# Kernel tuning notes

Hardware: AMD Instinct MI355X
Metric: run time of the kernel (lower is better)

The kernel has to match this reference:

```python
import jax, jax.numpy as jnp
import numpy as np


def setup_inputs() -> dict:
    key = jax.random.key(0)
    k1, k2 = jax.random.split(key)
    s = jax.random.normal(k1, (8192, 512), dtype=jnp.float32)
    t = jax.random.normal(k2, (8192, 512), dtype=jnp.float32)
    return {"s": s, "t": t}


def reference(s, t):
    # Pairwise squared Euclidean distance: dist[i, j] = ||t[j] - s[i]||^2
    # Expressed via the identity ||s||^2 + ||t||^2 - 2 s @ t^T to avoid
    # materializing the [n, q, d] broadcast intermediate of the original.
    s_sq = jnp.sum(s * s, axis=1)  # [n]
    t_sq = jnp.sum(t * t, axis=1)  # [q]
    cross = jnp.einsum('nd,qd->nq', s, t)  # [n, q]
    dist = s_sq[:, None] + t_sq[None, :] - 2.0 * cross
    return dist
```

## Files before the change

kernel.cpp:

```cpp
#include <hip/hip_runtime.h>
#include <hip/hip_bf16.h>
#include <stdint.h>


typedef __attribute__((ext_vector_type(8))) short short8v;
typedef __attribute__((ext_vector_type(4))) float f32x4;

static __device__ __forceinline__ unsigned short f32_to_bf16_rne(float f) {
    unsigned int u = __float_as_uint(f);
    unsigned int lsb = (u >> 16) & 1u;
    u += 0x7fffu + lsb;
    return (unsigned short)(u >> 16);
}

static __device__ __forceinline__ void async_load16(const void* g, void* l) {
    __builtin_amdgcn_global_load_lds(
        (const __attribute__((address_space(1))) void*)g,
        (__attribute__((address_space(3))) void*)l,
        16, 0, 0);
}

__global__ __launch_bounds__(256) void prep_kernel(const float* __restrict__ x,
                                                   unsigned short* __restrict__ xb,
                                                   float* __restrict__ nrm,
                                                   float scale) {
    const int tid  = threadIdx.x;
    const int wid  = tid >> 6;
    const int lane = tid & 63;
    const int row  = blockIdx.x * 4 + wid;
    const float* xr = x + (size_t)row * 512;

    float4 v0 = ((const float4*)xr)[lane * 2 + 0];
    float4 v1 = ((const float4*)xr)[lane * 2 + 1];

    float ss = v0.x * v0.x + v0.y * v0.y + v0.z * v0.z + v0.w * v0.w
             + v1.x * v1.x + v1.y * v1.y + v1.z * v1.z + v1.w * v1.w;
#pragma unroll
    for (int off = 32; off > 0; off >>= 1) ss += __shfl_down(ss, off, 64);
    if (lane == 0) nrm[row] = ss;

    unsigned short u[8];
    float vals[8] = {v0.x, v0.y, v0.z, v0.w, v1.x, v1.y, v1.z, v1.w};
#pragma unroll
    for (int e = 0; e < 8; ++e) u[e] = f32_to_bf16_rne(vals[e] * scale);
    unsigned int w0 = (unsigned)u[0] | ((unsigned)u[1] << 16);
    unsigned int w1 = (unsigned)u[2] | ((unsigned)u[3] << 16);
    unsigned int w2 = (unsigned)u[4] | ((unsigned)u[5] << 16);
    unsigned int w3 = (unsigned)u[6] | ((unsigned)u[7] << 16);
    uint4 pk = make_uint4(w0, w1, w2, w3);
    ((uint4*)(xb + (size_t)row * 512))[lane] = pk;
}

#define TILE 128
#define BK 64

__global__ __launch_bounds__(256) void dist_mfma(const unsigned short* __restrict__ sb,
                                                 const unsigned short* __restrict__ tb,
                                                 const float* __restrict__ ssq,
                                                 const float* __restrict__ tsq,
                                                 float* __restrict__ out,
                                                 int N, int Q, int D) {
    __shared__ unsigned short lds_a[TILE * BK];
    __shared__ unsigned short lds_b[TILE * BK];

    const int tid  = threadIdx.x;
    const int wid  = tid >> 6;
    const int lane = tid & 63;
    const int quad = lane >> 4;
    const int r    = lane & 15;

    const int bid = blockIdx.x;
    const int nBm = N / TILE, nBn = Q / TILE;
    int bm, bn;
    if ((nBm & 7) == 0 && (nBn & 7) == 0) {
        const int super = bid >> 6, within = bid & 63;
        const int spr = nBn >> 3;
        const int sm = super / spr, sn = super % spr;
        bm = (sm << 3) + (within >> 3);
        bn = (sn << 3) + (within & 7);
    } else {
        bm = bid / nBn;
        bn = bid - bm * nBn;
    }

    const int m_w = (wid & 1) * 64;
    const int n_w = (wid >> 1) * 64;

    f32x4 acc[4][4];
#pragma unroll
    for (int a = 0; a < 4; ++a)
#pragma unroll
        for (int b = 0; b < 4; ++b) acc[a][b] = (f32x4){0.f, 0.f, 0.f, 0.f};

    const unsigned short* gA[4];
    const unsigned short* gB[4];
    unsigned short* lA[4];
    unsigned short* lB[4];
#pragma unroll
    for (int i = 0; i < 4; ++i) {
        const int p    = i * 256 + tid;
        const int row  = p >> 3;
        const int gch  = (tid & 7) ^ (row & 7);
        gA[i] = sb + (size_t)(bm * TILE + row) * D + gch * 8;
        gB[i] = tb + (size_t)(bn * TILE + row) * D + gch * 8;
        lA[i] = lds_a + (i * 256 + wid * 64) * 8;
        lB[i] = lds_b + (i * 256 + wid * 64) * 8;
    }

    for (int k0 = 0; k0 < D; k0 += BK) {
        __syncthreads();
#pragma unroll
        for (int i = 0; i < 4; ++i) {
            async_load16(gA[i] + k0, lA[i]);
            async_load16(gB[i] + k0, lB[i]);
        }
        __syncthreads();

#pragma unroll
        for (int ks = 0; ks < 2; ++ks) {
            short8v aF[4], bF[4];
#pragma unroll
            for (int im = 0; im < 4; ++im) {
                const int row = m_w + im * 16 + r;
                const int cp  = (ks * 4 + quad) ^ (row & 7);
                aF[im] = *(const short8v*)(lds_a + row * BK + cp * 8);
            }
#pragma unroll
            for (int in = 0; in < 4; ++in) {
                const int row = n_w + in * 16 + r;
                const int cp  = (ks * 4 + quad) ^ (row & 7);
                bF[in] = *(const short8v*)(lds_b + row * BK + cp * 8);
            }
#pragma unroll
            for (int im = 0; im < 4; ++im)
#pragma unroll
                for (int in = 0; in < 4; ++in)
                    acc[im][in] = __builtin_amdgcn_mfma_f32_16x16x32_bf16(
                        aF[im], bF[in], acc[im][in], 0, 0, 0);
        }
    }

    const int gm = bm * TILE + m_w;
    const int gn = bn * TILE + n_w;
    float tq[4];
#pragma unroll
    for (int in = 0; in < 4; ++in) tq[in] = tsq[gn + in * 16 + r];
#pragma unroll
    for (int im = 0; im < 4; ++im) {
#pragma unroll
        for (int j = 0; j < 4; ++j) {
            const int i = gm + im * 16 + quad * 4 + j;
            const float sv = ssq[i];
            float* orow = out + (size_t)i * (size_t)Q + gn;
#pragma unroll
            for (int in = 0; in < 4; ++in)
                __builtin_nontemporal_store(sv + tq[in] + acc[im][in][j],
                                            &orow[in * 16 + r]);
        }
    }
}

__global__ void dist_fallback(const float* __restrict__ s, const float* __restrict__ t,
                              float* __restrict__ out, int N, int Q, int D) {
    __shared__ float ls[16][17], lt[16][17];
    const int tj = threadIdx.x, ti = threadIdx.y;
    const int i = blockIdx.y * 16 + ti, j = blockIdx.x * 16 + tj;
    float cross = 0.f, ssq = 0.f, tsq = 0.f;
    for (int k0 = 0; k0 < D; k0 += 16) {
        __syncthreads();
        ls[ti][tj] = s[(size_t)(blockIdx.y * 16 + ti) * D + k0 + tj];
        lt[ti][tj] = t[(size_t)(blockIdx.x * 16 + ti) * D + k0 + tj];
        __syncthreads();
#pragma unroll
        for (int kk = 0; kk < 16; ++kk) {
            float a = ls[ti][kk], b = lt[tj][kk];
            cross += a * b; ssq += a * a; tsq += b * b;
        }
    }
    out[(size_t)i * Q + j] = ssq + tsq - 2.f * cross;
}

extern "C" void kernel_launch(void* const* d_in, const int* in_sizes, int n_in,
                              void* d_out, int out_size, void* d_ws, size_t ws_size,
                              hipStream_t stream) {
    const float* s = (const float*)d_in[0];
    const float* t = (const float*)d_in[1];
    float* out = (float*)d_out;
    const int D = 512;
    const int N = in_sizes[0] / D;
    const int Q = in_sizes[1] / D;

    const size_t need = ((size_t)N + (size_t)Q) * D * sizeof(unsigned short)
                      + ((size_t)N + (size_t)Q) * sizeof(float);

    if (ws_size >= need && D == 512 && (N % TILE) == 0 && (Q % TILE) == 0) {
        unsigned short* sb = (unsigned short*)d_ws;
        unsigned short* tb = sb + (size_t)N * D;
        float* ssq = (float*)(tb + (size_t)Q * D);
        float* tsq = ssq + N;
        prep_kernel<<<N / 4, 256, 0, stream>>>(s, sb, ssq, -2.0f);
        prep_kernel<<<Q / 4, 256, 0, stream>>>(t, tb, tsq, 1.0f);
        const int blocks = (N / TILE) * (Q / TILE);
        dist_mfma<<<blocks, 256, 0, stream>>>(sb, tb, ssq, tsq, out, N, Q, D);
    } else {
        dim3 g(Q / 16, N / 16), b(16, 16);
        dist_fallback<<<g, b, 0, stream>>>(s, t, out, N, Q, D);
    }
}
```

Measured before the change: 347.9 us.

## Use 256x256 tiles with a 4-slot async LDS ring and prefetch depth two

Grows the block tile from 128x128 to 256x256 with 512 threads, so each wave computes a 128x64 sub-tile. The K step shrinks to 32, and global-to-LDS loads go into a 4-slot ring buffer issued two stages ahead. Explicit vmcnt waits plus one barrier per step replace the previous load-then-sync pattern, which stalled on every K step. MFMA priority is raised during the compute section; the risk is 128KB of LDS limiting occupancy to one block per CU, plus higher register use.

```diff
diff --git a/kernel.cpp b/kernel.cpp
--- a/kernel.cpp
+++ b/kernel.cpp
@@ -51,26 +51,30 @@
     ((uint4*)(xb + (size_t)row * 512))[lane] = pk;
 }
 
-#define TILE 128
-#define BK 64
-
-__global__ __launch_bounds__(256) void dist_mfma(const unsigned short* __restrict__ sb,
-                                                 const unsigned short* __restrict__ tb,
-                                                 const float* __restrict__ ssq,
-                                                 const float* __restrict__ tsq,
-                                                 float* __restrict__ out,
-                                                 int N, int Q, int D) {
-    __shared__ unsigned short lds_a[TILE * BK];
-    __shared__ unsigned short lds_b[TILE * BK];
+#define BM 256
+#define BK 32
+#define NSLOT 4
+
+__global__ __launch_bounds__(512, 2) void dist_mfma(const unsigned short* __restrict__ sb,
+                                                    const unsigned short* __restrict__ tb,
+                                                    const float* __restrict__ ssq,
+                                                    const float* __restrict__ tsq,
+                                                    float* __restrict__ out,
+                                                    int N, int Q, int D) {
+    __shared__ __align__(16) unsigned short lds[2 * NSLOT * 256 * 32];
 
     const int tid  = threadIdx.x;
     const int wid  = tid >> 6;
     const int lane = tid & 63;
     const int quad = lane >> 4;
     const int r    = lane & 15;
+    const int wr   = wid >> 2;
+    const int wc   = wid & 3;
+    const int m_w  = wr * 128;
+    const int n_w  = wc * 64;
 
     const int bid = blockIdx.x;
-    const int nBm = N / TILE, nBn = Q / TILE;
+    const int nBm = N / BM, nBn = Q / BM;
     int bm, bn;
     if ((nBm & 7) == 0 && (nBn & 7) == 0) {
         const int super = bid >> 6, within = bid & 63;
@@ -83,70 +87,83 @@
         bn = bid - bm * nBn;
     }
 
-    const int m_w = (wid & 1) * 64;
-    const int n_w = (wid >> 1) * 64;
-
-    f32x4 acc[4][4];
-#pragma unroll
-    for (int a = 0; a < 4; ++a)
+    f32x4 acc[8][4];
+#pragma unroll
+    for (int a = 0; a < 8; ++a)
 #pragma unroll
         for (int b = 0; b < 4; ++b) acc[a][b] = (f32x4){0.f, 0.f, 0.f, 0.f};
 
-    const unsigned short* gA[4];
-    const unsigned short* gB[4];
-    unsigned short* lA[4];
-    unsigned short* lB[4];
-#pragma unroll
-    for (int i = 0; i < 4; ++i) {
-        const int p    = i * 256 + tid;
-        const int row  = p >> 3;
-        const int gch  = (tid & 7) ^ (row & 7);
-        gA[i] = sb + (size_t)(bm * TILE + row) * D + gch * 8;
-        gB[i] = tb + (size_t)(bn * TILE + row) * D + gch * 8;
-        lA[i] = lds_a + (i * 256 + wid * 64) * 8;
-        lB[i] = lds_b + (i * 256 + wid * 64) * 8;
-    }
-
-    for (int k0 = 0; k0 < D; k0 += BK) {
-        __syncthreads();
-#pragma unroll
-        for (int i = 0; i < 4; ++i) {
-            async_load16(gA[i] + k0, lA[i]);
-            async_load16(gB[i] + k0, lB[i]);
-        }
-        __syncthreads();
-
-#pragma unroll
-        for (int ks = 0; ks < 2; ++ks) {
-            short8v aF[4], bF[4];
-#pragma unroll
-            for (int im = 0; im < 4; ++im) {
-                const int row = m_w + im * 16 + r;
-                const int cp  = (ks * 4 + quad) ^ (row & 7);
-                aF[im] = *(const short8v*)(lds_a + row * BK + cp * 8);
-            }
-#pragma unroll
-            for (int in = 0; in < 4; ++in) {
-                const int row = n_w + in * 16 + r;
-                const int cp  = (ks * 4 + quad) ^ (row & 7);
-                bF[in] = *(const short8v*)(lds_b + row * BK + cp * 8);
-            }
-#pragma unroll
-            for (int im = 0; im < 4; ++im)
-#pragma unroll
-                for (int in = 0; in < 4; ++in)
-                    acc[im][in] = __builtin_amdgcn_mfma_f32_16x16x32_bf16(
-                        aF[im], bF[in], acc[im][in], 0, 0, 0);
-        }
-    }
-
-    const int gm = bm * TILE + m_w;
-    const int gn = bn * TILE + n_w;
+    const unsigned short* gA[2];
+    const unsigned short* gB[2];
+    unsigned short* lA[2];
+    unsigned short* lB[2];
+#pragma unroll
+    for (int i = 0; i < 2; ++i) {
+        const int p   = i * 512 + tid;
+        const int row = p >> 2;
+        const int gch = (p & 3) ^ (row & 3);
+        gA[i] = sb + (size_t)(bm * BM + row) * D + gch * 8;
+        gB[i] = tb + (size_t)(bn * BM + row) * D + gch * 8;
+        lA[i] = lds + (i * 512 + wid * 64) * 8;
+        lB[i] = lds + NSLOT * 8192 + (i * 512 + wid * 64) * 8;
+    }
+
+#define STAGE(t, s) do { const int k0_ = (t) * BK;                  \
+        async_load16(gA[0] + k0_, lA[0] + (s) * 8192);              \
+        async_load16(gB[0] + k0_, lB[0] + (s) * 8192);              \
+        async_load16(gA[1] + k0_, lA[1] + (s) * 8192);              \
+        async_load16(gB[1] + k0_, lB[1] + (s) * 8192); } while (0)
+
+    STAGE(0, 0);
+    STAGE(1, 1);
+
+    const int NT = D / BK;
+    for (int t = 0; t < NT; ++t) {
+        if (t + 2 < NT) STAGE(t + 2, (t + 2) & 3);
+        if (t < NT - 2) {
+            asm volatile("s_waitcnt vmcnt(8) lgkmcnt(0)" ::: "memory");
+        } else if (t == NT - 2) {
+            asm volatile("s_waitcnt vmcnt(4) lgkmcnt(0)" ::: "memory");
+        } else {
+            asm volatile("s_waitcnt vmcnt(0) lgkmcnt(0)" ::: "memory");
+        }
+        __builtin_amdgcn_sched_barrier(0);
+        __builtin_amdgcn_s_barrier();
+        __builtin_amdgcn_sched_barrier(0);
+
+        const unsigned short* ba = lds + (t & 3) * 8192;
+        const unsigned short* bb = lds + NSLOT * 8192 + (t & 3) * 8192;
+        short8v aF[8], bF[4];
+#pragma unroll
+        for (int im = 0; im < 8; ++im) {
+            const int row = m_w + im * 16 + r;
+            const int cp  = quad ^ (row & 3);
+            aF[im] = *(const short8v*)(ba + row * 32 + cp * 8);
+        }
+#pragma unroll
+        for (int in = 0; in < 4; ++in) {
+            const int row = n_w + in * 16 + r;
+            const int cp  = quad ^ (row & 3);
+            bF[in] = *(const short8v*)(bb + row * 32 + cp * 8);
+        }
+        __builtin_amdgcn_s_setprio(1);
+#pragma unroll
+        for (int im = 0; im < 8; ++im)
+#pragma unroll
+            for (int in = 0; in < 4; ++in)
+                acc[im][in] = __builtin_amdgcn_mfma_f32_16x16x32_bf16(
+                    aF[im], bF[in], acc[im][in], 0, 0, 0);
+        __builtin_amdgcn_s_setprio(0);
+    }
+#undef STAGE
+
+    const int gm = bm * BM + m_w;
+    const int gn = bn * BM + n_w;
     float tq[4];
 #pragma unroll
     for (int in = 0; in < 4; ++in) tq[in] = tsq[gn + in * 16 + r];
 #pragma unroll
-    for (int im = 0; im < 4; ++im) {
+    for (int im = 0; im < 8; ++im) {
 #pragma unroll
         for (int j = 0; j < 4; ++j) {
             const int i = gm + im * 16 + quad * 4 + j;
@@ -193,15 +210,15 @@
     const size_t need = ((size_t)N + (size_t)Q) * D * sizeof(unsigned short)
                       + ((size_t)N + (size_t)Q) * sizeof(float);
 
-    if (ws_size >= need && D == 512 && (N % TILE) == 0 && (Q % TILE) == 0) {
+    if (ws_size >= need && D == 512 && (N % BM) == 0 && (Q % BM) == 0) {
         unsigned short* sb = (unsigned short*)d_ws;
         unsigned short* tb = sb + (size_t)N * D;
         float* ssq = (float*)(tb + (size_t)Q * D);
         float* tsq = ssq + N;
         prep_kernel<<<N / 4, 256, 0, stream>>>(s, sb, ssq, -2.0f);
         prep_kernel<<<Q / 4, 256, 0, stream>>>(t, tb, tsq, 1.0f);
-        const int blocks = (N / TILE) * (Q / TILE);
-        dist_mfma<<<blocks, 256, 0, stream>>>(sb, tb, ssq, tsq, out, N, Q, D);
+        const int blocks = (N / BM) * (Q / BM);
+        dist_mfma<<<blocks, 512, 0, stream>>>(sb, tb, ssq, tsq, out, N, Q, D);
     } else {
         dim3 g(Q / 16, N / 16), b(16, 16);
         dist_fallback<<<g, b, 0, stream>>>(s, t, out, N, Q, D);
```

Result: slower. 370.6 us (+6.5%).

## Drop LDS staging and load MFMA fragments directly from global memory

Applied to the files above, without the earlier changes.

Removes the LDS staging path and all block barriers. Each wave now loads its bf16 A and B fragments straight from global memory into registers and computes a 64x128 sub-tile, inside a 256x128 block tile. Block order is remapped into 8 contiguous regions, apparently one per XCD, to improve L2 locality. This trades explicit shared-memory reuse across waves for reliance on L1/L2 caches, and adds register pressure from 32 accumulators, with launch bounds asking for 2 blocks per CU.

```diff
diff --git a/kernel.cpp b/kernel.cpp
--- a/kernel.cpp
+++ b/kernel.cpp
@@ -11,13 +11,6 @@
     unsigned int lsb = (u >> 16) & 1u;
     u += 0x7fffu + lsb;
     return (unsigned short)(u >> 16);
-}
-
-static __device__ __forceinline__ void async_load16(const void* g, void* l) {
-    __builtin_amdgcn_global_load_lds(
-        (const __attribute__((address_space(1))) void*)g,
-        (__attribute__((address_space(3))) void*)l,
-        16, 0, 0);
 }
 
 __global__ __launch_bounds__(256) void prep_kernel(const float* __restrict__ x,
@@ -51,18 +44,16 @@
     ((uint4*)(xb + (size_t)row * 512))[lane] = pk;
 }
 
-#define TILE 128
-#define BK 64
+#define BM 256
+#define BN 128
 
-__global__ __launch_bounds__(256) void dist_mfma(const unsigned short* __restrict__ sb,
-                                                 const unsigned short* __restrict__ tb,
-                                                 const float* __restrict__ ssq,
-                                                 const float* __restrict__ tsq,
-                                                 float* __restrict__ out,
-                                                 int N, int Q, int D) {
-    __shared__ unsigned short lds_a[TILE * BK];
-    __shared__ unsigned short lds_b[TILE * BK];
 
+__global__ __launch_bounds__(256, 2) void dist_mfma(const unsigned short* __restrict__ sb,
+                                                    const unsigned short* __restrict__ tb,
+                                                    const float* __restrict__ ssq,
+                                                    const float* __restrict__ tsq,
+                                                    float* __restrict__ out,
+                                                    int N, int Q, int D) {
     const int tid  = threadIdx.x;
     const int wid  = tid >> 6;
     const int lane = tid & 63;
@@ -70,81 +61,56 @@
     const int r    = lane & 15;
 
     const int bid = blockIdx.x;
-    const int nBm = N / TILE, nBn = Q / TILE;
+    const int nBm = N / BM, nBn = Q / BN;
     int bm, bn;
-    if ((nBm & 7) == 0 && (nBn & 7) == 0) {
-        const int super = bid >> 6, within = bid & 63;
-        const int spr = nBn >> 3;
-        const int sm = super / spr, sn = super % spr;
-        bm = (sm << 3) + (within >> 3);
-        bn = (sn << 3) + (within & 7);
+    if (nBm == 32 && nBn == 64) {
+        const int c = bid & 7;
+        const int w = bid >> 3;
+        bm = (c >> 2) * 16 + (w >> 4);
+        bn = (c & 3) * 16 + (w & 15);
     } else {
         bm = bid / nBn;
         bn = bid - bm * nBn;
     }
 
-    const int m_w = (wid & 1) * 64;
-    const int n_w = (wid >> 1) * 64;
+    const int gm = bm * BM + wid * 64;
+    const int gn = bn * BN;
 
-    f32x4 acc[4][4];
+    const unsigned short* aP[4];
+    const unsigned short* bP[8];
+#pragma unroll
+    for (int im = 0; im < 4; ++im)
+        aP[im] = sb + (size_t)(gm + im * 16 + r) * 512 + quad * 8;
+#pragma unroll
+    for (int in = 0; in < 8; ++in)
+        bP[in] = tb + (size_t)(gn + in * 16 + r) * 512 + quad * 8;
+
+    f32x4 acc[4][8];
 #pragma unroll
     for (int a = 0; a < 4; ++a)
 #pragma unroll
-        for (int b = 0; b < 4; ++b) acc[a][b] = (f32x4){0.f, 0.f, 0.f, 0.f};
+        for (int b = 0; b < 8; ++b) acc[a][b] = (f32x4){0.f, 0.f, 0.f, 0.f};
 
-    const unsigned short* gA[4];
-    const unsigned short* gB[4];
-    unsigned short* lA[4];
-    unsigned short* lB[4];
+#pragma unroll 4
+    for (int t = 0; t < 16; ++t) {
+        short8v aF[4], bF[8];
 #pragma unroll
-    for (int i = 0; i < 4; ++i) {
-        const int p    = i * 256 + tid;
-        const int row  = p >> 3;
-        const int gch  = (tid & 7) ^ (row & 7);
-        gA[i] = sb + (size_t)(bm * TILE + row) * D + gch * 8;
-        gB[i] = tb + (size_t)(bn * TILE + row) * D + gch * 8;
-        lA[i] = lds_a + (i * 256 + wid * 64) * 8;
-        lB[i] = lds_b + (i * 256 + wid * 64) * 8;
+        for (int im = 0; im < 4; ++im)
+            aF[im] = *(const short8v*)(aP[im] + t * 32);
+#pragma unroll
+        for (int in = 0; in < 8; ++in)
+            bF[in] = *(const short8v*)(bP[in] + t * 32);
+#pragma unroll
+        for (int im = 0; im < 4; ++im)
+#pragma unroll
+            for (int in = 0; in < 8; ++in)
+                acc[im][in] = __builtin_amdgcn_mfma_f32_16x16x32_bf16(
+                    aF[im], bF[in], acc[im][in], 0, 0, 0);
     }
 
-    for (int k0 = 0; k0 < D; k0 += BK) {
-        __syncthreads();
+    float tq[8];
 #pragma unroll
-        for (int i = 0; i < 4; ++i) {
-            async_load16(gA[i] + k0, lA[i]);
-            async_load16(gB[i] + k0, lB[i]);
-        }
-        __syncthreads();
-
-#pragma unroll
-        for (int ks = 0; ks < 2; ++ks) {
-            short8v aF[4], bF[4];
-#pragma unroll
-            for (int im = 0; im < 4; ++im) {
-                const int row = m_w + im * 16 + r;
-                const int cp  = (ks * 4 + quad) ^ (row & 7);
-                aF[im] = *(const short8v*)(lds_a + row * BK + cp * 8);
-            }
-#pragma unroll
-            for (int in = 0; in < 4; ++in) {
-                const int row = n_w + in * 16 + r;
-                const int cp  = (ks * 4 + quad) ^ (row & 7);
-                bF[in] = *(const short8v*)(lds_b + row * BK + cp * 8);
-            }
-#pragma unroll
-            for (int im = 0; im < 4; ++im)
-#pragma unroll
-                for (int in = 0; in < 4; ++in)
-                    acc[im][in] = __builtin_amdgcn_mfma_f32_16x16x32_bf16(
-                        aF[im], bF[in], acc[im][in], 0, 0, 0);
-        }
-    }
-
-    const int gm = bm * TILE + m_w;
-    const int gn = bn * TILE + n_w;
-    float tq[4];
-#pragma unroll
-    for (int in = 0; in < 4; ++in) tq[in] = tsq[gn + in * 16 + r];
+    for (int in = 0; in < 8; ++in) tq[in] = tsq[gn + in * 16 + r];
 #pragma unroll
     for (int im = 0; im < 4; ++im) {
 #pragma unroll
@@ -153,7 +119,7 @@
             const float sv = ssq[i];
             float* orow = out + (size_t)i * (size_t)Q + gn;
 #pragma unroll
-            for (int in = 0; in < 4; ++in)
+            for (int in = 0; in < 8; ++in)
                 __builtin_nontemporal_store(sv + tq[in] + acc[im][in][j],
                                             &orow[in * 16 + r]);
         }
@@ -193,14 +159,14 @@
     const size_t need = ((size_t)N + (size_t)Q) * D * sizeof(unsigned short)
                       + ((size_t)N + (size_t)Q) * sizeof(float);
 
-    if (ws_size >= need && D == 512 && (N % TILE) == 0 && (Q % TILE) == 0) {
+    if (ws_size >= need && D == 512 && (N % BM) == 0 && (Q % BN) == 0) {
         unsigned short* sb = (unsigned short*)d_ws;
         unsigned short* tb = sb + (size_t)N * D;
         float* ssq = (float*)(tb + (size_t)Q * D);
         float* tsq = ssq + N;
         prep_kernel<<<N / 4, 256, 0, stream>>>(s, sb, ssq, -2.0f);
         prep_kernel<<<Q / 4, 256, 0, stream>>>(t, tb, tsq, 1.0f);
-        const int blocks = (N / TILE) * (Q / TILE);
+        const int blocks = (N / BM) * (Q / BN);
         dist_mfma<<<blocks, 256, 0, stream>>>(sb, tb, ssq, tsq, out, N, Q, D);
     } else {
         dim3 g(Q / 16, N / 16), b(16, 16);
```

Result: slower. 459.8 us (+32.2%).
